# Optimization experiments

Hardware: AMD Instinct MI355X
Metric: run time of the kernel (lower is better)

Reference implementation:

```python
import jax, jax.numpy as jnp
import numpy as np

B, CIN, H, W = 8, 128, 64, 64
COUT, KH, KW = 128, 3, 3
STRIDE = (1, 1)
PAD = (1, 1)
DIL = (1, 1)
GROUPS = 1
OFFSET_GROUPS = 1

def _out_size(i, k, s, p, d):
    return (i + 2 * p - d * (k - 1) - 1) // s + 1

HO = _out_size(H, KH, STRIDE[0], PAD[0], DIL[0])
WO = _out_size(W, KW, STRIDE[1], PAD[1], DIL[1])


def setup_inputs() -> dict:
    key = jax.random.key(0)
    k1, k2, k3, k4 = jax.random.split(key, 4)
    x = jax.random.normal(k1, (B, CIN, H, W), jnp.float32)
    offset = jax.random.normal(k2, (B, 2 * OFFSET_GROUPS * KH * KW, HO, WO), jnp.float32)
    fan_in = (CIN // GROUPS) * KH * KW
    bound = 1.0 / np.sqrt(fan_in)
    weight = jax.random.uniform(k3, (COUT, CIN // GROUPS, KH, KW), jnp.float32, -bound, bound)
    bias = jax.random.uniform(k4, (COUT,), jnp.float32, -bound, bound)
    return {"x": x, "offset": offset, "weight": weight, "bias": bias}


def _deform_conv2d(x, offset, weight, bias):
    Bn, Cin, Hi, Wi = x.shape
    K = KH * KW
    Goff, Gw = OFFSET_GROUPS, GROUPS
    Cpg = Cin // Goff

    # base sampling positions (before learned offsets)
    ys = jnp.arange(HO, dtype=jnp.float32) * STRIDE[0] - PAD[0]  # [HO]
    xs = jnp.arange(WO, dtype=jnp.float32) * STRIDE[1] - PAD[1]  # [WO]
    base_y = jnp.repeat(jnp.arange(KH, dtype=jnp.float32) * DIL[0], KW)  # [K]
    base_x = jnp.tile(jnp.arange(KW, dtype=jnp.float32) * DIL[1], KH)    # [K]

    # offsets: channel layout is 2*(g*K + k) + {0: dy, 1: dx}
    off = offset.reshape(Bn, Goff, K, 2, HO, WO)
    py = base_y[None, None, :, None, None] + ys[None, None, None, :, None] + off[:, :, :, 0]  # [B,Goff,K,HO,WO]
    px = base_x[None, None, :, None, None] + xs[None, None, None, None, :] + off[:, :, :, 1]

    y0 = jnp.floor(py)
    x0 = jnp.floor(px)
    ly = py - y0  # fractional weights
    lx = px - x0

    xg = x.reshape(Bn, Goff, Cpg, Hi * Wi)

    def gather_one(img, lin):  # img [Cpg, H*W], lin [K,HO,WO] -> [Cpg,K,HO,WO]
        return img[:, lin]

    gather = jax.vmap(jax.vmap(gather_one))  # over B and Goff

    def corner(yi, xi, w):
        # zero-padding semantics: out-of-bounds corner contributes 0
        mask = (yi >= 0) & (yi < Hi) & (xi >= 0) & (xi < Wi)
        iy = jnp.clip(yi, 0, Hi - 1).astype(jnp.int32)
        ix = jnp.clip(xi, 0, Wi - 1).astype(jnp.int32)
        lin = iy * Wi + ix  # [B,Goff,K,HO,WO]
        wm = (w * mask.astype(x.dtype))[:, :, None]  # broadcast over channel axis
        return gather(xg, lin) * wm  # [B,Goff,Cpg,K,HO,WO]

    val = (corner(y0, x0, (1 - ly) * (1 - lx))
           + corner(y0, x0 + 1, (1 - ly) * lx)
           + corner(y0 + 1, x0, ly * (1 - lx))
           + corner(y0 + 1, x0 + 1, ly * lx))  # [B,Goff,Cpg,K,HO,WO]

    # grouped conv accumulate
    val = val.reshape(Bn, Gw, Cin // Gw, K, HO, WO)
    wg = weight.reshape(Gw, COUT // Gw, Cin // Gw, K)
    out = jnp.einsum('bgckhw,gock->bgohw', val, wg).reshape(Bn, COUT, HO, WO)
    return out + bias[None, :, None, None]


def reference(x, offset, weight, bias):
    return _deform_conv2d(x, offset, weight, bias)
```

## Files before the change

### kernel.cpp

```cpp
#include <hip/hip_runtime.h>

typedef unsigned int   u32;
typedef unsigned short u16;
typedef short bf16x8 __attribute__((ext_vector_type(8)));
typedef float f32x4  __attribute__((ext_vector_type(4)));

#define CIN   128
#define COUT  128
#define Hh    64
#define Ww    64
#define Bb    8
#define KPOS  9
#define NSS   9
#define PLANE 1288
#define XT_ELEMS (Bb*Hh*Ww*CIN)

__device__ __forceinline__ float bflo(u32 u){ return __uint_as_float(u << 16); }
__device__ __forceinline__ float bfhi(u32 u){ return __uint_as_float(u & 0xffff0000u); }

__device__ __forceinline__ u32 packbf(float a, float b){
    u32 ua = __float_as_uint(a);
    u32 ub = __float_as_uint(b);
    ua += 0x7fffu + ((ua >> 16) & 1u);
    ub += 0x7fffu + ((ub >> 16) & 1u);
    return (ua >> 16) | (ub & 0xffff0000u);
}
__device__ __forceinline__ u16 tobf(float a){
    u32 ua = __float_as_uint(a);
    ua += 0x7fffu + ((ua >> 16) & 1u);
    return (u16)(ua >> 16);
}

__global__ __launch_bounds__(256) void k_prep(const float* __restrict__ x,
                                              const float* __restrict__ w,
                                              u16* __restrict__ xT,
                                              u16* __restrict__ Wt){
    __shared__ float tile[32*33];
    int bi  = blockIdx.x;
    int tid = threadIdx.x;
    if (bi < 4096){
        int st = bi & 127, ct = (bi >> 7) & 3, b = bi >> 9;
        int sb = st * 32, cb = ct * 32;
        int i = tid >> 5, j = tid & 31;
        const float* xp = x + ((size_t)(b*CIN + cb) * 4096) + sb;
#pragma unroll
        for (int rr = 0; rr < 4; ++rr){
            int ci = i + rr*8;
            tile[ci*33 + j] = xp[(size_t)ci*4096 + j];
        }
        __syncthreads();
        int ii = tid >> 4, jj = tid & 15;
        u32* outp = (u32*)xT + ((size_t)b*4096 + sb)*64 + (cb >> 1) + jj;
#pragma unroll
        for (int rr = 0; rr < 2; ++rr){
            int sl = ii + rr*16;
            float v0 = tile[(2*jj  )*33 + sl];
            float v1 = tile[(2*jj+1)*33 + sl];
            outp[(size_t)sl*64] = packbf(v0, v1);
        }
    } else {
        int gid = (bi - 4096)*256 + tid;
        int jf   = gid & 7;
        int lane = (gid >> 3) & 63;
        int mt   = (gid >> 9) & 7;
        int kt   = gid >> 12;
        int m  = mt*16 + (lane & 15);
        int kk = (lane >> 4)*8 + jf;
        int ck = kt*32 + kk;
        int kpos = ck >> 7;
        int cin  = ck & 127;
        Wt[gid] = tobf(w[((size_t)m*128 + cin)*9 + kpos]);
    }
}

__global__ __launch_bounds__(256, 2)
void k_main(const float* __restrict__ off, const float* __restrict__ bias,
            const u16* __restrict__ xT, const u16* __restrict__ Wt,
            float* __restrict__ out){
    __shared__ u32 Vsm[2][4*PLANE];

    int tid = threadIdx.x;
    int bi  = blockIdx.x;
    int b   = bi & 7;
    int t   = bi >> 3;
    int s0  = t * 64;

    int p  = tid >> 2, qt = tid & 3;
    int ho = t;
    int wo = p;
    const u16* xb_base = xT + (size_t)b * (Hh*Ww*CIN) + qt*32;

    int lane = tid & 63, wave = tid >> 6;
    int wm = wave >> 1, wn = wave & 1;
    int quad = lane >> 4, l16 = lane & 15;

    f32x4 acc[4][2];
#pragma unroll
    for (int i = 0; i < 4; ++i)
#pragma unroll
        for (int j = 0; j < 2; ++j) acc[i][j] = {0.f, 0.f, 0.f, 0.f};

    int   aa[4];
    float wt[4];
    float dyr, dxr;
    uint4 q[16];
    uint4 araw[2][4];

    auto off_load = [&](int kpos){
        size_t ob = ((size_t)(b*18 + 2*kpos))*4096 + (s0 + p);
        dyr = off[ob];
        dxr = off[ob + 4096];
    };
    auto state_calc = [&](int kpos){
        int kh = kpos / 3, kw = kpos - kh*3;
        float py = (float)(ho + kh - 1) + dyr;
        float px = (float)(wo + kw - 1) + dxr;
        float y0f = floorf(py), x0f = floorf(px);
        float ly = py - y0f, lx = px - x0f;
        int y0 = (int)y0f, x0 = (int)x0f;
        int y1 = y0 + 1,  x1 = x0 + 1;
        float my0 = (y0 >= 0 && y0 < Hh) ? 1.f : 0.f;
        float my1 = (y1 >= 0 && y1 < Hh) ? 1.f : 0.f;
        float mx0 = (x0 >= 0 && x0 < Ww) ? 1.f : 0.f;
        float mx1 = (x1 >= 0 && x1 < Ww) ? 1.f : 0.f;
        float omly = 1.f - ly, omlx = 1.f - lx;
        wt[0] = omly*omlx*my0*mx0;
        wt[1] = omly*lx  *my0*mx1;
        wt[2] = ly  *omlx*my1*mx0;
        wt[3] = ly  *lx  *my1*mx1;
        int cy0 = min(max(y0,0),Hh-1), cy1 = min(max(y1,0),Hh-1);
        int cx0 = min(max(x0,0),Ww-1), cx1 = min(max(x1,0),Ww-1);
        aa[0] = (cy0*Ww + cx0)*CIN;
        aa[1] = (cy0*Ww + cx1)*CIN;
        aa[2] = (cy1*Ww + cx0)*CIN;
        aa[3] = (cy1*Ww + cx1)*CIN;
    };
    auto gather = [&](){
#pragma unroll
        for (int c = 0; c < 4; ++c){
            const u16* s = xb_base + aa[c];
#pragma unroll
            for (int u = 0; u < 4; ++u)
                q[c*4 + u] = *(const uint4*)(s + u*8);
        }
    };
    auto blend_store = [&](int buf){
        u32* dst = &Vsm[buf][qt*PLANE + p*20];
#pragma unroll
        for (int u = 0; u < 4; ++u){
            u32 res[4];
#pragma unroll
            for (int d = 0; d < 4; ++d){
                float lo = 0.f, hi = 0.f;
#pragma unroll
                for (int c = 0; c < 4; ++c){
                    u32 v = ((const u32*)&q[c*4 + u])[d];
                    lo = fmaf(wt[c], bflo(v), lo);
                    hi = fmaf(wt[c], bfhi(v), hi);
                }
                res[d] = packbf(lo, hi);
            }
            *(uint4*)(dst + u*4) = *(const uint4*)res;
        }
    };
    auto loadA = [&](int ks, uint4 a[4]){
#pragma unroll
        for (int i = 0; i < 4; ++i)
            a[i] = *(const uint4*)(Wt + (size_t)(((ks*8 + wm*4 + i)*64 + lane))*8);
    };

    off_load(0);
    state_calc(0);
    gather();
    loadA(0, araw[0]);

    for (int kp = 0; kp < NSS; ++kp){
        bool have_nxt = (kp + 1 < NSS);
        if (have_nxt) off_load(kp + 1);
        blend_store(kp & 1);
        if (have_nxt){
            state_calc(kp + 1);
            gather();
        }
        __syncthreads();

#pragma unroll
        for (int ks2 = 0; ks2 < 4; ++ks2){
            int flat = kp*4 + ks2;
            if (flat < 35) loadA(flat + 1, araw[(ks2+1) & 1]);
            uint4 braw[2];
#pragma unroll
            for (int j = 0; j < 2; ++j)
                braw[j] = *(const uint4*)&Vsm[kp & 1][ks2*PLANE + ((wn*2 + j)*16 + l16)*20 + quad*4];
#pragma unroll
            for (int i = 0; i < 4; ++i){
                bf16x8 av = __builtin_bit_cast(bf16x8, araw[ks2 & 1][i]);
#pragma unroll
                for (int j = 0; j < 2; ++j){
                    bf16x8 bv = __builtin_bit_cast(bf16x8, braw[j]);
                    acc[i][j] = __builtin_amdgcn_mfma_f32_16x16x32_bf16(av, bv, acc[i][j], 0, 0, 0);
                }
            }
        }
    }

#pragma unroll
    for (int i = 0; i < 4; ++i){
        int cout0 = (wm*4 + i)*16 + quad*4;
#pragma unroll
        for (int j = 0; j < 2; ++j){
            int pcol = (wn*2 + j)*16 + l16;
            size_t obase = ((size_t)(b*COUT + cout0))*4096 + (s0 + pcol);
#pragma unroll
            for (int r = 0; r < 4; ++r){
                out[obase + (size_t)r*4096] = acc[i][j][r] + bias[cout0 + r];
            }
        }
    }
}

extern "C" void kernel_launch(void* const* d_in, const int* in_sizes, int n_in,
                              void* d_out, int out_size, void* d_ws, size_t ws_size,
                              hipStream_t stream){
    const float* x    = (const float*)d_in[0];
    const float* off  = (const float*)d_in[1];
    const float* w    = (const float*)d_in[2];
    const float* bias = (const float*)d_in[3];
    float* out = (float*)d_out;

    u16* xT = (u16*)d_ws;
    u16* Wt = xT + XT_ELEMS;

    k_prep<<<dim3(4672), dim3(256), 0, stream>>>(x, w, xT, Wt);
    k_main<<<dim3(512),  dim3(256), 0, stream>>>(off, bias, xT, Wt, out);
}
```

Measured before the change: 107.8 us.

## Switch bf16 staging to fp16 with packed half blending and interleaved channel gather

```diff
diff --git a/kernel.cpp b/kernel.cpp
--- a/kernel.cpp
+++ b/kernel.cpp
@@ -2,7 +2,8 @@
 
 typedef unsigned int   u32;
 typedef unsigned short u16;
-typedef short bf16x8 __attribute__((ext_vector_type(8)));
+typedef _Float16 f16x8 __attribute__((ext_vector_type(8)));
+typedef _Float16 f16x2 __attribute__((ext_vector_type(2)));
 typedef float f32x4  __attribute__((ext_vector_type(4)));
 
 #define CIN   128
@@ -15,20 +16,13 @@
 #define PLANE 1288
 #define XT_ELEMS (Bb*Hh*Ww*CIN)
 
-__device__ __forceinline__ float bflo(u32 u){ return __uint_as_float(u << 16); }
-__device__ __forceinline__ float bfhi(u32 u){ return __uint_as_float(u & 0xffff0000u); }
-
-__device__ __forceinline__ u32 packbf(float a, float b){
-    u32 ua = __float_as_uint(a);
-    u32 ub = __float_as_uint(b);
-    ua += 0x7fffu + ((ua >> 16) & 1u);
-    ub += 0x7fffu + ((ub >> 16) & 1u);
-    return (ua >> 16) | (ub & 0xffff0000u);
-}
-__device__ __forceinline__ u16 tobf(float a){
-    u32 ua = __float_as_uint(a);
-    ua += 0x7fffu + ((ua >> 16) & 1u);
-    return (u16)(ua >> 16);
+__device__ __forceinline__ u32 packh(float a, float b){
+    f16x2 t = { (_Float16)a, (_Float16)b };
+    return __builtin_bit_cast(u32, t);
+}
+__device__ __forceinline__ u16 tof16(float a){
+    _Float16 h = (_Float16)a;
+    return __builtin_bit_cast(u16, h);
 }
 
 __global__ __launch_bounds__(256) void k_prep(const float* __restrict__ x,
@@ -56,7 +50,7 @@
             int sl = ii + rr*16;
             float v0 = tile[(2*jj  )*33 + sl];
             float v1 = tile[(2*jj+1)*33 + sl];
-            outp[(size_t)sl*64] = packbf(v0, v1);
+            outp[(size_t)sl*64] = packh(v0, v1);
         }
     } else {
         int gid = (bi - 4096)*256 + tid;
@@ -69,7 +63,7 @@
         int ck = kt*32 + kk;
         int kpos = ck >> 7;
         int cin  = ck & 127;
-        Wt[gid] = tobf(w[((size_t)m*128 + cin)*9 + kpos]);
+        Wt[gid] = tof16(w[((size_t)m*128 + cin)*9 + kpos]);
     }
 }
 
@@ -85,10 +79,10 @@
     int t   = bi >> 3;
     int s0  = t * 64;
 
-    int p  = tid >> 2, qt = tid & 3;
+    int p  = tid >> 2, sub = tid & 3;
     int ho = t;
     int wo = p;
-    const u16* xb_base = xT + (size_t)b * (Hh*Ww*CIN) + qt*32;
+    const u16* xb_base = xT + (size_t)b * (Hh*Ww*CIN) + sub*8;
 
     int lane = tid & 63, wave = tid >> 6;
     int wm = wave >> 1, wn = wave & 1;
@@ -103,7 +97,7 @@
     int   aa[4];
     float wt[4];
     float dyr, dxr;
-    uint4 q[16];
+    uint4 q[4][4];
     uint4 araw[2][4];
 
     auto off_load = [&](int kpos){
@@ -140,27 +134,32 @@
         for (int c = 0; c < 4; ++c){
             const u16* s = xb_base + aa[c];
 #pragma unroll
-            for (int u = 0; u < 4; ++u)
-                q[c*4 + u] = *(const uint4*)(s + u*8);
+            for (int k = 0; k < 4; ++k)
+                q[c][k] = *(const uint4*)(s + k*32);
         }
     };
     auto blend_store = [&](int buf){
-        u32* dst = &Vsm[buf][qt*PLANE + p*20];
-#pragma unroll
-        for (int u = 0; u < 4; ++u){
+        f16x2 w2[4];
+#pragma unroll
+        for (int c = 0; c < 4; ++c){
+            _Float16 h = (_Float16)wt[c];
+            w2[c] = (f16x2){h, h};
+        }
+        u32* dst = &Vsm[buf][p*20 + sub*4];
+#pragma unroll
+        for (int k = 0; k < 4; ++k){
             u32 res[4];
 #pragma unroll
             for (int d = 0; d < 4; ++d){
-                float lo = 0.f, hi = 0.f;
+                f16x2 a2 = {(_Float16)0.f, (_Float16)0.f};
 #pragma unroll
                 for (int c = 0; c < 4; ++c){
-                    u32 v = ((const u32*)&q[c*4 + u])[d];
-                    lo = fmaf(wt[c], bflo(v), lo);
-                    hi = fmaf(wt[c], bfhi(v), hi);
+                    f16x2 v = __builtin_bit_cast(f16x2, ((const u32*)&q[c][k])[d]);
+                    a2 = w2[c]*v + a2;
                 }
-                res[d] = packbf(lo, hi);
+                res[d] = __builtin_bit_cast(u32, a2);
             }
-            *(uint4*)(dst + u*4) = *(const uint4*)res;
+            *(uint4*)(dst + k*PLANE) = *(const uint4*)res;
         }
     };
     auto loadA = [&](int ks, uint4 a[4]){
@@ -194,11 +193,11 @@
                 braw[j] = *(const uint4*)&Vsm[kp & 1][ks2*PLANE + ((wn*2 + j)*16 + l16)*20 + quad*4];
 #pragma unroll
             for (int i = 0; i < 4; ++i){
-                bf16x8 av = __builtin_bit_cast(bf16x8, araw[ks2 & 1][i]);
+                f16x8 av = __builtin_bit_cast(f16x8, araw[ks2 & 1][i]);
 #pragma unroll
                 for (int j = 0; j < 2; ++j){
-                    bf16x8 bv = __builtin_bit_cast(bf16x8, braw[j]);
-                    acc[i][j] = __builtin_amdgcn_mfma_f32_16x16x32_bf16(av, bv, acc[i][j], 0, 0, 0);
+                    f16x8 bv = __builtin_bit_cast(f16x8, braw[j]);
+                    acc[i][j] = __builtin_amdgcn_mfma_f32_16x16x32_f16(av, bv, acc[i][j], 0, 0, 0);
                 }
             }
         }
```

Result: faster. 100.8 us (-6.5%).
